# Performance work log

Measured on AMD Instinct MI355X. Metric: run time of the kernel, lower is better.

The kernel has to match this reference:

```python
import jax, jax.numpy as jnp
import numpy as np

DRUG_NUM, DIS_NUM, HIDE_DIM = 60000, 40000, 128
HOPS, N_LAYERS, N_HEADS, FFN_DIM, N_EDGES = 7, 2, 4, 512, 800000
N_NODES = DRUG_NUM + DIS_NUM


def _ln(x, s, b, eps=1e-5):
    m = jnp.mean(x, axis=-1, keepdims=True)
    v = jnp.var(x, axis=-1, keepdims=True)
    return (x - m) * jax.lax.rsqrt(v + eps) * s + b


def setup_inputs() -> dict:
    ks = jax.random.split(jax.random.key(0), 16)
    L, D, F = N_LAYERS, HIDE_DIM, FFN_DIM
    sd = 0.05  # param init scale
    n = lambda k, shape, s=sd: jax.random.normal(k, shape, jnp.float32) * s
    kk = jax.random.split(ks[15], 12)
    return {
        'ifTraining': 0,
        'uid': jax.random.randint(ks[0], (256,), 0, DRUG_NUM, jnp.int64 if jax.config.jax_enable_x64 else jnp.int32),
        'iid': jax.random.randint(ks[1], (256,), 0, DIS_NUM, jnp.int64 if jax.config.jax_enable_x64 else jnp.int32),
        'norm': 1,
        'drug_emb': n(ks[2], (DRUG_NUM, D), 0.1),
        'dis_emb': n(ks[3], (DIS_NUM, D), 0.1),
        'edge_src': jax.random.randint(ks[4], (N_EDGES,), 0, N_NODES, jnp.int32),
        'edge_dst': jax.random.randint(ks[5], (N_EDGES,), 0, N_NODES, jnp.int32),
        'edge_val': jax.random.uniform(ks[6], (N_EDGES,), jnp.float32) * 0.1,  # normalized adj values
        'att_w': n(ks[7], (D, D)), 'att_b': jnp.zeros((D,), jnp.float32),
        'ln1_s': jnp.ones((L, D), jnp.float32), 'ln1_b': jnp.zeros((L, D), jnp.float32),
        'q_w': n(kk[0], (L, D, D)), 'q_b': jnp.zeros((L, D), jnp.float32),
        'k_w': n(kk[1], (L, D, D)), 'k_b': jnp.zeros((L, D), jnp.float32),
        'v_w': n(kk[2], (L, D, D)), 'v_b': jnp.zeros((L, D), jnp.float32),
        'o_w': n(kk[3], (L, D, D)), 'o_b': jnp.zeros((L, D), jnp.float32),
        'ln2_s': jnp.ones((L, D), jnp.float32), 'ln2_b': jnp.zeros((L, D), jnp.float32),
        'f1_w': n(kk[4], (L, D, F)), 'f1_b': jnp.zeros((L, F), jnp.float32),
        'f2_w': n(kk[5], (L, F, D)), 'f2_b': jnp.zeros((L, D), jnp.float32),
        'fln_s': jnp.ones((D,), jnp.float32), 'fln_b': jnp.zeros((D,), jnp.float32),
        'attn_w': n(kk[6], (2 * D, 1)), 'attn_b': jnp.zeros((1,), jnp.float32),
    }


def reference(ifTraining, uid, iid, norm, drug_emb, dis_emb, edge_src, edge_dst, edge_val,
              att_w, att_b, ln1_s, ln1_b, q_w, q_b, k_w, k_b, v_w, v_b, o_w, o_b,
              ln2_s, ln2_b, f1_w, f1_b, f2_w, f2_b, fln_s, fln_b, attn_w, attn_b):
    N, D, S, dh = N_NODES, HIDE_DIM, HOPS + 1, HIDE_DIM // N_HEADS
    # ---- re_features: K sparse-adjacency hops over concatenated embeddings ----
    x = jnp.concatenate([drug_emb, dis_emb], axis=0)  # [N, D]
    feats = [x]
    for _ in range(HOPS):
        msgs = x[edge_src] * edge_val[:, None]          # [E, D] gather
        x = jax.ops.segment_sum(msgs, edge_dst, num_segments=N)  # [N, D] scatter-add
        feats.append(x)
    nf = jnp.stack(feats, axis=1)                        # [N, S, D]
    # ---- graph-transformer over the hop sequence (eval: dropout = identity) ----
    h = nf @ att_w + att_b                               # [N, S, D]
    for l in range(N_LAYERS):
        y = _ln(h, ln1_s[l], ln1_b[l])
        q = (y @ q_w[l] + q_b[l]).reshape(N, S, N_HEADS, dh)
        k = (y @ k_w[l] + k_b[l]).reshape(N, S, N_HEADS, dh)
        v = (y @ v_w[l] + v_b[l]).reshape(N, S, N_HEADS, dh)
        a = jnp.einsum('nshd,nthd->nhst', q, k) * (dh ** -0.5)
        a = jax.nn.softmax(a, axis=-1)                   # [N, H, S, S]
        y = jnp.einsum('nhst,nthd->nshd', a, v).reshape(N, S, D)
        h = h + (y @ o_w[l] + o_b[l])
        y = _ln(h, ln2_s[l], ln2_b[l])
        h = h + (jax.nn.gelu(y @ f1_w[l] + f1_b[l]) @ f2_w[l] + f2_b[l])
    out = _ln(h, fln_s, fln_b)
    # ---- readout: node token + softmax attention over hop tokens ----
    node = out[:, 0, :]                                  # [N, D]
    neigh = out[:, 1:, :]                                # [N, HOPS, D]
    target = jnp.broadcast_to(node[:, None, :], neigh.shape)
    att = jnp.concatenate([target, neigh], axis=-1) @ attn_w + attn_b  # [N, HOPS, 1]
    att = jax.nn.softmax(att, axis=1)
    final = node + jnp.sum(neigh * att, axis=1)          # [N, D]
    return final[:DRUG_NUM], final[DRUG_NUM:]
```

## Files before the change

kernel.cpp:

```cpp
#include <hip/hip_runtime.h>
#include <hip/hip_bf16.h>

typedef __hip_bfloat16 bf16;
typedef __attribute__((ext_vector_type(8))) short s16x8;
typedef __attribute__((ext_vector_type(4))) float f32x4;

#define NDRUG 60000
#define NDIS  40000
#define NN    100000
#define DIM   128
#define NHOPS 7
#define NEDGE 800000
#define NSB   98

__device__ __forceinline__ float u2f(unsigned short u) {
    union { unsigned int i; float f; } c; c.i = ((unsigned int)u) << 16; return c.f;
}
__device__ __forceinline__ ushort f2u(float f) {
    bf16 h = __float2bfloat16(f);
    return *reinterpret_cast<ushort*>(&h);
}


__global__ void k_init(const float* __restrict__ drug, const float* __restrict__ dis,
                       ushort* __restrict__ nf) {
    int i = blockIdx.x * 256 + threadIdx.x;
    if (i >= NN * 32) return;
    int n = i >> 5, g = (i & 31) << 2;
    const float* sp = (n < NDRUG) ? drug + (size_t)n * 128 + g
                                  : dis + (size_t)(n - NDRUG) * 128 + g;
    float4 v = *(const float4*)sp;
    ushort4 o;
    o.x = f2u(v.x); o.y = f2u(v.y); o.z = f2u(v.z); o.w = f2u(v.w);
    *(ushort4*)(nf + (size_t)n * 1024 + g) = o;
}

__global__ void k_count(const int* __restrict__ edst, int* __restrict__ cnt) {
    int e = blockIdx.x * 256 + threadIdx.x;
    if (e < NEDGE) atomicAdd(&cnt[edst[e]], 1);
}

__global__ void k_scanA(const int* __restrict__ cnt, int* __restrict__ incl,
                        int* __restrict__ btot) {
    __shared__ int part[1024];
    int b = blockIdx.x, t = threadIdx.x;
    int i = b * 1024 + t;
    part[t] = (i < NN) ? cnt[i] : 0;
    __syncthreads();
    for (int o = 1; o < 1024; o <<= 1) {
        int u = (t >= o) ? part[t - o] : 0;
        __syncthreads();
        part[t] += u;
        __syncthreads();
    }
    if (i < NN) incl[i] = part[t];
    if (t == 1023) btot[b] = part[1023];
}

__global__ void k_scanB(const int* __restrict__ btot, int* __restrict__ boff) {
    if (threadIdx.x == 0) {
        int run = 0;
        for (int b = 0; b < NSB; b++) { boff[b] = run; run += btot[b]; }
        boff[NSB] = run;
    }
}

__global__ void k_scanC(const int* __restrict__ cnt, const int* __restrict__ incl,
                        const int* __restrict__ boff, int* __restrict__ rp) {
    int i = blockIdx.x * 256 + threadIdx.x;
    if (i < NN) rp[i] = incl[i] - cnt[i] + boff[i >> 10];
    if (i == 0) rp[NN] = boff[NSB];
}

__global__ void k_copyrp(const int* __restrict__ rp, int* __restrict__ cur) {
    int i = blockIdx.x * 256 + threadIdx.x;
    if (i < NN) cur[i] = rp[i];
}

__global__ void k_scatter(const int* __restrict__ esrc, const int* __restrict__ edst,
                          const float* __restrict__ eval, int* __restrict__ cur,
                          int* __restrict__ ssrc, float* __restrict__ sval) {
    int e = blockIdx.x * 256 + threadIdx.x;
    if (e >= NEDGE) return;
    int d = edst[e];
    int pos = atomicAdd(&cur[d], 1);
    ssrc[pos] = esrc[e];
    sval[pos] = eval[e];
}

__global__ void k_hopg(ushort* __restrict__ nf, const int* __restrict__ rp,
                       const int* __restrict__ ssrc, const float* __restrict__ sval, int s) {
    int t = blockIdx.x * 256 + threadIdx.x;
    if (t >= NN * 32) return;
    int n = t >> 5, d0 = (t & 31) << 2;
    int e0 = rp[n], e1 = rp[n + 1];
    float4 a = make_float4(0.f, 0.f, 0.f, 0.f);
    for (int e = e0; e < e1; e++) {
        int src = ssrc[e];
        float val = sval[e];
        ushort4 u = *(const ushort4*)(nf + (size_t)src * 1024 + (size_t)(s - 1) * 128 + d0);
        a.x += u2f(u.x) * val; a.y += u2f(u.y) * val;
        a.z += u2f(u.z) * val; a.w += u2f(u.w) * val;
    }
    ushort4 o;
    o.x = f2u(a.x); o.y = f2u(a.y); o.z = f2u(a.z); o.w = f2u(a.w);
    *(ushort4*)(nf + (size_t)n * 1024 + (size_t)s * 128 + d0) = o;
}


__global__ void k_pack(const float* __restrict__ W, ushort* __restrict__ P, int K, int Nout) {
    int idx = blockIdx.x * 256 + threadIdx.x;
    int tot = (Nout >> 4) * (K >> 3) * 16;
    if (idx >= tot) return;
    int c = idx & 15;
    int r = idx >> 4;
    int kb = r % (K >> 3);
    int nt = r / (K >> 3);
    ushort o[8];
    #pragma unroll
    for (int i = 0; i < 8; i++)
        o[i] = f2u(W[(size_t)(kb * 8 + i) * Nout + nt * 16 + c]);
    uint4 v;
    v.x = (uint)o[0] | ((uint)o[1] << 16);
    v.y = (uint)o[2] | ((uint)o[3] << 16);
    v.z = (uint)o[4] | ((uint)o[5] << 16);
    v.w = (uint)o[6] | ((uint)o[7] << 16);
    *(uint4*)(P + (size_t)idx * 8) = v;
}

__global__ void k_catb(const float* __restrict__ qb, const float* __restrict__ kb,
                       const float* __restrict__ vb, float* __restrict__ o) {
    int i = threadIdx.x;
    o[i] = (i < 128) ? qb[i] : ((i < 256) ? kb[i - 128] : vb[i - 256]);
}


template <int ACT, int ADD, int OUTBF, int NTPW>
__global__ void k_mgemm(const ushort* __restrict__ X, const ushort* __restrict__ Wp,
                        const float* __restrict__ bias, void* __restrict__ Yv,
                        int M, int K, int Nout) {
    int w = threadIdx.x >> 6, lane = threadIdx.x & 63;
    int lr = lane & 15, lg = lane >> 4;
    int m0 = blockIdx.x * 16;
    int kb8 = K >> 3;
    int row = m0 + lr; if (row > M - 1) row = M - 1;
    const ushort* ap = X + (size_t)row * K + lg * 8;
    f32x4 acc[NTPW] = {};
    for (int k0 = 0; k0 < K; k0 += 32, ap += 32) {
        s16x8 af = *(const s16x8*)ap;
        int kb = (k0 >> 3) + lg;
        #pragma unroll
        for (int t = 0; t < NTPW; t++) {
            int nt = w + t * 4;
            const ushort* bp = Wp + (((size_t)nt * kb8 + kb) * 16 + lr) * 8;
            s16x8 bf_ = *(const s16x8*)bp;
            acc[t] = __builtin_amdgcn_mfma_f32_16x16x32_bf16(af, bf_, acc[t], 0, 0, 0);
        }
    }
    #pragma unroll
    for (int t = 0; t < NTPW; t++) {
        int n = (w + t * 4) * 16 + lr;
        float bv = bias[n];
        #pragma unroll
        for (int j = 0; j < 4; j++) {
            int m = m0 + lg * 4 + j;
            if (m >= M) continue;
            float v = acc[t][j] + bv;
            if (ACT == 1) {
                float x = v;
                float z = 0.7978845608028654f * (x + 0.044715f * x * x * x);
                v = x / (1.0f + __expf(-2.0f * z));
            }
            if (OUTBF) {
                ((ushort*)Yv)[(size_t)m * Nout + n] = f2u(v);
            } else if (ADD) {
                ((float*)Yv)[(size_t)m * Nout + n] += v;
            } else {
                ((float*)Yv)[(size_t)m * Nout + n] = v;
            }
        }
    }
}


__global__ void k_lnqkvattnO(float* __restrict__ H, const ushort* __restrict__ Wqkv,
                             const ushort* __restrict__ Wo, const float* __restrict__ sc,
                             const float* __restrict__ bi, const float* __restrict__ bqkv,
                             const float* __restrict__ bo, int M) {
    __shared__ ushort ylds[16][136];
    __shared__ ushort big[16][392];
    __shared__ float  as_[2][256];
    int w = threadIdx.x >> 6, lane = threadIdx.x & 63;
    int lr = lane & 15, lg = lane >> 4;
    int m0 = blockIdx.x * 16;

    #pragma unroll
    for (int i = 0; i < 4; i++) {
        int row = w * 4 + i;
        int grow = m0 + row; if (grow > M - 1) grow = M - 1;
        float2 x = *(const float2*)(H + (size_t)grow * 128 + lane * 2);
        float sum = x.x + x.y, sq = x.x * x.x + x.y * x.y;
        #pragma unroll
        for (int o = 32; o; o >>= 1) { sum += __shfl_xor(sum, o); sq += __shfl_xor(sq, o); }
        float mean = sum * (1.f / 128.f);
        float inv = rsqrtf(sq * (1.f / 128.f) - mean * mean + 1e-5f);
        float y0 = (x.x - mean) * inv * sc[lane * 2 + 0] + bi[lane * 2 + 0];
        float y1 = (x.y - mean) * inv * sc[lane * 2 + 1] + bi[lane * 2 + 1];
        *(uint*)&ylds[row][lane * 2] = (uint)f2u(y0) | ((uint)f2u(y1) << 16);
    }
    __syncthreads();

    {
        f32x4 acc[6] = {};
        for (int k0 = 0; k0 < 128; k0 += 32) {
            s16x8 af = *(const s16x8*)&ylds[lr][lg * 8 + k0];
            int kb = (k0 >> 3) + lg;
            #pragma unroll
            for (int t = 0; t < 6; t++) {
                int nt = w + t * 4;
                const ushort* bp = Wqkv + (((size_t)nt * 16 + kb) * 16 + lr) * 8;
                s16x8 bf_ = *(const s16x8*)bp;
                acc[t] = __builtin_amdgcn_mfma_f32_16x16x32_bf16(af, bf_, acc[t], 0, 0, 0);
            }
        }
        #pragma unroll
        for (int t = 0; t < 6; t++) {
            int n = (w + t * 4) * 16 + lr;
            float bv = bqkv[n];
            #pragma unroll
            for (int j = 0; j < 4; j++) big[lg * 4 + j][n] = f2u(acc[t][j] + bv);
        }
    }
    __syncthreads();

    if (w < 2) {
        int hh = lane >> 4, s_ = (lane >> 1) & 7, p = lane & 1;
        const float scale = 0.17677669529663687f;
        float dots[4];
        float mx = -1e30f;
        #pragma unroll
        for (int t4 = 0; t4 < 4; t4++) {
            int t = p * 4 + t4;
            float dot = 0.f;
            #pragma unroll
            for (int d = 0; d < 32; d++)
                dot += u2f(big[w * 8 + s_][hh * 32 + d]) * u2f(big[w * 8 + t][128 + hh * 32 + d]);
            dots[t4] = dot * scale;
            mx = fmaxf(mx, dots[t4]);
        }
        mx = fmaxf(mx, __shfl_xor(mx, 1));
        float sum = 0.f, e4[4];
        #pragma unroll
        for (int t4 = 0; t4 < 4; t4++) { e4[t4] = __expf(dots[t4] - mx); sum += e4[t4]; }
        sum += __shfl_xor(sum, 1);
        float rinv = 1.f / sum;
        #pragma unroll
        for (int t4 = 0; t4 < 4; t4++) as_[w][hh * 64 + s_ * 8 + p * 4 + t4] = e4[t4] * rinv;
    }
    __syncthreads();

    if (w < 2) {
        #pragma unroll
        for (int i = 0; i < 16; i++) {
            int o = i * 64 + lane;
            int ss = o >> 7, rem = o & 127, h2 = rem >> 5, dd = rem & 31;
            float accv = 0.f;
            #pragma unroll
            for (int t = 0; t < 8; t++)
                accv += as_[w][h2 * 64 + ss * 8 + t] * u2f(big[w * 8 + t][256 + h2 * 32 + dd]);
            ylds[w * 8 + ss][rem] = f2u(accv);
        }
    }
    __syncthreads();

    {
        f32x4 acc[2] = {};
        for (int k0 = 0; k0 < 128; k0 += 32) {
            s16x8 af = *(const s16x8*)&ylds[lr][lg * 8 + k0];
            int kb = (k0 >> 3) + lg;
            #pragma unroll
            for (int t = 0; t < 2; t++) {
                int nt = w + t * 4;
                const ushort* bp = Wo + (((size_t)nt * 16 + kb) * 16 + lr) * 8;
                s16x8 bf_ = *(const s16x8*)bp;
                acc[t] = __builtin_amdgcn_mfma_f32_16x16x32_bf16(af, bf_, acc[t], 0, 0, 0);
            }
        }
        #pragma unroll
        for (int t = 0; t < 2; t++) {
            int n = (w + t * 4) * 16 + lr;
            float bv = bo[n];
            #pragma unroll
            for (int j = 0; j < 4; j++) {
                int m = m0 + lg * 4 + j;
                if (m >= M) continue;
                H[(size_t)m * 128 + n] += acc[t][j] + bv;
            }
        }
    }
}


__global__ void k_lnffn(float* __restrict__ H, const ushort* __restrict__ Wf1,
                        const ushort* __restrict__ Wf2, const float* __restrict__ sc,
                        const float* __restrict__ bi, const float* __restrict__ b1,
                        const float* __restrict__ b2, int M) {
    __shared__ ushort ylds[16][136];
    __shared__ ushort big[16][520];
    int w = threadIdx.x >> 6, lane = threadIdx.x & 63;
    int lr = lane & 15, lg = lane >> 4;
    int m0 = blockIdx.x * 16;

    #pragma unroll
    for (int i = 0; i < 4; i++) {
        int row = w * 4 + i;
        int grow = m0 + row; if (grow > M - 1) grow = M - 1;
        float2 x = *(const float2*)(H + (size_t)grow * 128 + lane * 2);
        float sum = x.x + x.y, sq = x.x * x.x + x.y * x.y;
        #pragma unroll
        for (int o = 32; o; o >>= 1) { sum += __shfl_xor(sum, o); sq += __shfl_xor(sq, o); }
        float mean = sum * (1.f / 128.f);
        float inv = rsqrtf(sq * (1.f / 128.f) - mean * mean + 1e-5f);
        float y0 = (x.x - mean) * inv * sc[lane * 2 + 0] + bi[lane * 2 + 0];
        float y1 = (x.y - mean) * inv * sc[lane * 2 + 1] + bi[lane * 2 + 1];
        *(uint*)&ylds[row][lane * 2] = (uint)f2u(y0) | ((uint)f2u(y1) << 16);
    }
    __syncthreads();

    {
        f32x4 acc[8] = {};
        for (int k0 = 0; k0 < 128; k0 += 32) {
            s16x8 af = *(const s16x8*)&ylds[lr][lg * 8 + k0];
            int kb = (k0 >> 3) + lg;
            #pragma unroll
            for (int t = 0; t < 8; t++) {
                int nt = w + t * 4;
                const ushort* bp = Wf1 + (((size_t)nt * 16 + kb) * 16 + lr) * 8;
                s16x8 bf_ = *(const s16x8*)bp;
                acc[t] = __builtin_amdgcn_mfma_f32_16x16x32_bf16(af, bf_, acc[t], 0, 0, 0);
            }
        }
        #pragma unroll
        for (int t = 0; t < 8; t++) {
            int n = (w + t * 4) * 16 + lr;
            float bv = b1[n];
            #pragma unroll
            for (int j = 0; j < 4; j++) {
                float x = acc[t][j] + bv;
                float z = 0.7978845608028654f * (x + 0.044715f * x * x * x);
                big[lg * 4 + j][n] = f2u(x / (1.0f + __expf(-2.0f * z)));
            }
        }
    }
    __syncthreads();

    {
        f32x4 acc[2] = {};
        for (int k0 = 0; k0 < 512; k0 += 32) {
            s16x8 af = *(const s16x8*)&big[lr][lg * 8 + k0];
            int kb = (k0 >> 3) + lg;
            #pragma unroll
            for (int t = 0; t < 2; t++) {
                int nt = w + t * 4;
                const ushort* bp = Wf2 + (((size_t)nt * 64 + kb) * 16 + lr) * 8;
                s16x8 bf_ = *(const s16x8*)bp;
                acc[t] = __builtin_amdgcn_mfma_f32_16x16x32_bf16(af, bf_, acc[t], 0, 0, 0);
            }
        }
        #pragma unroll
        for (int t = 0; t < 2; t++) {
            int n = (w + t * 4) * 16 + lr;
            float bv = b2[n];
            #pragma unroll
            for (int j = 0; j < 4; j++) {
                int m = m0 + lg * 4 + j;
                if (m >= M) continue;
                H[(size_t)m * 128 + n] += acc[t][j] + bv;
            }
        }
    }
}


__global__ void k_pool(const float* __restrict__ Hc, const float* __restrict__ fs,
                       const float* __restrict__ fb, const float* __restrict__ aw,
                       const float* __restrict__ ab, float* __restrict__ out,
                       int Nc, int n0g) {
    int w = threadIdx.x >> 6, lane = threadIdx.x & 63;
    int nl = blockIdx.x * 4 + w;
    if (nl >= Nc) return;
    const float* hp = Hc + (size_t)nl * 1024;
    float s0 = fs[lane * 2], s1 = fs[lane * 2 + 1];
    float b0 = fb[lane * 2], b1 = fb[lane * 2 + 1];
    float2 yl[8];
    #pragma unroll
    for (int s = 0; s < 8; s++) {
        float2 x = *(const float2*)(hp + s * DIM + lane * 2);
        float sum = x.x + x.y, sq = x.x * x.x + x.y * x.y;
        #pragma unroll
        for (int o = 32; o; o >>= 1) { sum += __shfl_xor(sum, o); sq += __shfl_xor(sq, o); }
        float mean = sum * (1.f / 128.f);
        float inv = rsqrtf(sq * (1.f / 128.f) - mean * mean + 1e-5f);
        yl[s].x = (x.x - mean) * inv * s0 + b0;
        yl[s].y = (x.y - mean) * inv * s1 + b1;
    }
    float awn0 = aw[lane * 2], awn1 = aw[lane * 2 + 1];
    float awh0 = aw[128 + lane * 2], awh1 = aw[128 + lane * 2 + 1];
    float abv = ab[0];
    float lg[7];
    #pragma unroll
    for (int s = 0; s < 7; s++) {
        float part = yl[0].x * awn0 + yl[0].y * awn1 + yl[s + 1].x * awh0 + yl[s + 1].y * awh1;
        #pragma unroll
        for (int o = 32; o; o >>= 1) part += __shfl_xor(part, o);
        lg[s] = part + abv;
    }
    float mx = lg[0];
    #pragma unroll
    for (int s = 1; s < 7; s++) mx = fmaxf(mx, lg[s]);
    float sum = 0.f;
    #pragma unroll
    for (int s = 0; s < 7; s++) { lg[s] = __expf(lg[s] - mx); sum += lg[s]; }
    float rinv = 1.f / sum;
    float2 f = yl[0];
    #pragma unroll
    for (int s = 0; s < 7; s++) { f.x += lg[s] * rinv * yl[s + 1].x; f.y += lg[s] * rinv * yl[s + 1].y; }
    size_t ob = (size_t)(n0g + nl) * DIM + lane * 2;
    out[ob + 0] = f.x;
    out[ob + 1] = f.y;
}


extern "C" void kernel_launch(void* const* d_in, const int* in_sizes, int n_in,
                              void* d_out, int out_size, void* d_ws, size_t ws_size,
                              hipStream_t stream) {
    const float* drug  = (const float*)d_in[4];
    const float* dis   = (const float*)d_in[5];
    const int*   esrc  = (const int*)d_in[6];
    const int*   edst  = (const int*)d_in[7];
    const float* eval  = (const float*)d_in[8];
    const float* att_w = (const float*)d_in[9];
    const float* att_b = (const float*)d_in[10];
    const float* ln1_s = (const float*)d_in[11];
    const float* ln1_b = (const float*)d_in[12];
    const float* q_w   = (const float*)d_in[13];
    const float* q_b   = (const float*)d_in[14];
    const float* k_w   = (const float*)d_in[15];
    const float* k_b   = (const float*)d_in[16];
    const float* v_w   = (const float*)d_in[17];
    const float* v_b   = (const float*)d_in[18];
    const float* o_w   = (const float*)d_in[19];
    const float* o_b   = (const float*)d_in[20];
    const float* ln2_s = (const float*)d_in[21];
    const float* ln2_b = (const float*)d_in[22];
    const float* f1_w  = (const float*)d_in[23];
    const float* f1_b  = (const float*)d_in[24];
    const float* f2_w  = (const float*)d_in[25];
    const float* f2_b  = (const float*)d_in[26];
    const float* fln_s = (const float*)d_in[27];
    const float* fln_b = (const float*)d_in[28];
    const float* aw    = (const float*)d_in[29];
    const float* ab    = (const float*)d_in[30];
    float* out = (float*)d_out;

    char* ws = (char*)d_ws;
    size_t nfB = (size_t)NN * 1024 * 2;
    ushort* nf = (ushort*)ws;
    size_t off = (nfB + 255) & ~(size_t)255;

    ushort* wpk = (ushort*)(ws + off);
    size_t offCsr = off + (1 << 20);
    int*   rp   = (int*)(ws + offCsr);
    int*   cnt  = rp + (NN + 1);
    int*   ssrc = cnt + NN;
    float* sval = (float*)(ssrc + NEDGE);
    int*   incl = (int*)(sval + NEDGE);
    int*   btot = incl + NN;
    int*   boff = btot + 128;
    size_t csrInts = (size_t)(NN + 1) + NN + NEDGE + NEDGE + NN + 256;
    size_t off2 = offCsr + ((csrInts * 4 + 255) & ~(size_t)255);

    size_t scratchB = (ws_size > off2) ? ws_size - off2 : 0;
    long long ncMax = (long long)(scratchB / 4096);
    ncMax &= ~1LL;
    if (ncMax < 2) ncMax = 2;
    int Nc = (int)((ncMax < NN) ? ncMax : NN);
    int nchunks = (NN + Nc - 1) / Nc;
    Nc = (NN + nchunks - 1) / nchunks;
    if (Nc & 1) Nc++;
    size_t U = (size_t)Nc * 4096;
    float* hbuf = (float*)(ws + off2);

    size_t wpAtt = 0;
    size_t wpQKV[2], wpO[2], wpF1[2], wpF2[2];
    {
        size_t p = 16384;
        for (int l = 0; l < 2; l++) {
            wpQKV[l] = p; p += 49152;
            wpO[l]   = p; p += 16384;
            wpF1[l]  = p; p += 65536;
            wpF2[l]  = p; p += 65536;
        }
    }
    float* qkvB = (float*)(wpk + 409600);

    {
        int b128 = (16384 / 8 + 255) / 256;
        int b512 = (65536 / 8 + 255) / 256;
        k_pack<<<b128, 256, 0, stream>>>(att_w, wpk + wpAtt, 128, 128);
        for (int l = 0; l < 2; l++) {
            k_pack<<<b128, 256, 0, stream>>>(q_w + (size_t)l * 16384, wpk + wpQKV[l], 128, 128);
            k_pack<<<b128, 256, 0, stream>>>(k_w + (size_t)l * 16384, wpk + wpQKV[l] + 16384, 128, 128);
            k_pack<<<b128, 256, 0, stream>>>(v_w + (size_t)l * 16384, wpk + wpQKV[l] + 32768, 128, 128);
            k_pack<<<b128, 256, 0, stream>>>(o_w + (size_t)l * 16384, wpk + wpO[l], 128, 128);
            k_pack<<<b512, 256, 0, stream>>>(f1_w + (size_t)l * 65536, wpk + wpF1[l], 128, 512);
            k_pack<<<b512, 256, 0, stream>>>(f2_w + (size_t)l * 65536, wpk + wpF2[l], 512, 128);
            k_catb<<<1, 384, 0, stream>>>(q_b + l * 128, k_b + l * 128, v_b + l * 128, qkvB + l * 384);
        }
    }

    (void)hipMemsetAsync(cnt, 0, (size_t)NN * 4, stream);
    k_count<<<(NEDGE + 255) / 256, 256, 0, stream>>>(edst, cnt);
    k_scanA<<<NSB, 1024, 0, stream>>>(cnt, incl, btot);
    k_scanB<<<1, 64, 0, stream>>>(btot, boff);
    k_scanC<<<(NN + 255) / 256, 256, 0, stream>>>(cnt, incl, boff, rp);
    k_copyrp<<<(NN + 255) / 256, 256, 0, stream>>>(rp, cnt);
    k_scatter<<<(NEDGE + 255) / 256, 256, 0, stream>>>(esrc, edst, eval, cnt, ssrc, sval);

    k_init<<<(NN * 32 + 255) / 256, 256, 0, stream>>>(drug, dis, nf);
    for (int s = 1; s <= NHOPS; s++)
        k_hopg<<<(NN * 32 + 255) / 256, 256, 0, stream>>>(nf, rp, ssrc, sval, s);

    for (int c = 0; c < nchunks; c++) {
        int cn0 = c * Nc;
        int cn = NN - cn0; if (cn > Nc) cn = Nc;
        if (cn <= 0) break;
        int Mc = cn * 8;
        int mb = (Mc + 15) / 16;
        int nb = (cn + 3) / 4;

        k_mgemm<0, 0, 0, 2><<<mb, 256, 0, stream>>>(nf + (size_t)cn0 * 1024, wpk + wpAtt,
                                                    att_b, hbuf, Mc, 128, 128);
        for (int l = 0; l < 2; l++) {
            k_lnqkvattnO<<<mb, 256, 0, stream>>>(hbuf, wpk + wpQKV[l], wpk + wpO[l],
                                                 ln1_s + l * 128, ln1_b + l * 128,
                                                 qkvB + l * 384, o_b + l * 128, Mc);
            k_lnffn<<<mb, 256, 0, stream>>>(hbuf, wpk + wpF1[l], wpk + wpF2[l],
                                            ln2_s + l * 128, ln2_b + l * 128,
                                            f1_b + l * 512, f2_b + l * 128, Mc);
        }
        k_pool<<<nb, 256, 0, stream>>>(hbuf, fln_s, fln_b, aw, ab, out, cn, cn0);
    }
    (void)in_sizes; (void)n_in; (void)out_size;
}
```

Measured before the change: 3.045 ms.

## Fuse attention and FFN sublayers into one per-layer kernel with LDS-resident residual

Merges the LN+QKV+attention+O kernel and the LN+FFN kernel into a single k_layer kernel. Each block loads its 16 residual rows into shared memory once, applies both sublayer residual updates there, and writes them back once. This removes one launch per layer and the global round trip of the residual stream between the two sublayers. In exchange, shared memory per block grows (an extra 16x132 float tile and a larger big buffer), which may lower occupancy.

```diff
diff --git a/kernel.cpp b/kernel.cpp
--- a/kernel.cpp
+++ b/kernel.cpp
@@ -183,29 +183,43 @@
 }
 
 
-__global__ void k_lnqkvattnO(float* __restrict__ H, const ushort* __restrict__ Wqkv,
-                             const ushort* __restrict__ Wo, const float* __restrict__ sc,
-                             const float* __restrict__ bi, const float* __restrict__ bqkv,
-                             const float* __restrict__ bo, int M) {
+__global__ void k_layer(float* __restrict__ H,
+                        const ushort* __restrict__ Wqkv, const ushort* __restrict__ Wo,
+                        const ushort* __restrict__ Wf1, const ushort* __restrict__ Wf2,
+                        const float* __restrict__ s1v, const float* __restrict__ b1v,
+                        const float* __restrict__ bqkv, const float* __restrict__ bo,
+                        const float* __restrict__ s2v, const float* __restrict__ b2v,
+                        const float* __restrict__ bf1, const float* __restrict__ bf2,
+                        int M) {
+    __shared__ float  h[16][132];
     __shared__ ushort ylds[16][136];
-    __shared__ ushort big[16][392];
+    __shared__ ushort big[16][520];
     __shared__ float  as_[2][256];
-    int w = threadIdx.x >> 6, lane = threadIdx.x & 63;
+    int tid = threadIdx.x;
+    int w = tid >> 6, lane = tid & 63;
     int lr = lane & 15, lg = lane >> 4;
     int m0 = blockIdx.x * 16;
 
     #pragma unroll
+    for (int i = 0; i < 2; i++) {
+        int gi = i * 256 + tid;
+        int row = gi >> 5, c4 = (gi & 31) << 2;
+        int grow = m0 + row; if (grow > M - 1) grow = M - 1;
+        *(float4*)&h[row][c4] = *(const float4*)(H + (size_t)grow * 128 + c4);
+    }
+    __syncthreads();
+
+    #pragma unroll
     for (int i = 0; i < 4; i++) {
         int row = w * 4 + i;
-        int grow = m0 + row; if (grow > M - 1) grow = M - 1;
-        float2 x = *(const float2*)(H + (size_t)grow * 128 + lane * 2);
+        float2 x = *(const float2*)&h[row][lane * 2];
         float sum = x.x + x.y, sq = x.x * x.x + x.y * x.y;
         #pragma unroll
         for (int o = 32; o; o >>= 1) { sum += __shfl_xor(sum, o); sq += __shfl_xor(sq, o); }
         float mean = sum * (1.f / 128.f);
         float inv = rsqrtf(sq * (1.f / 128.f) - mean * mean + 1e-5f);
-        float y0 = (x.x - mean) * inv * sc[lane * 2 + 0] + bi[lane * 2 + 0];
-        float y1 = (x.y - mean) * inv * sc[lane * 2 + 1] + bi[lane * 2 + 1];
+        float y0 = (x.x - mean) * inv * s1v[lane * 2 + 0] + b1v[lane * 2 + 0];
+        float y1 = (x.y - mean) * inv * s1v[lane * 2 + 1] + b1v[lane * 2 + 1];
         *(uint*)&ylds[row][lane * 2] = (uint)f2u(y0) | ((uint)f2u(y1) << 16);
     }
     __syncthreads();
@@ -291,38 +305,22 @@
             int n = (w + t * 4) * 16 + lr;
             float bv = bo[n];
             #pragma unroll
-            for (int j = 0; j < 4; j++) {
-                int m = m0 + lg * 4 + j;
-                if (m >= M) continue;
-                H[(size_t)m * 128 + n] += acc[t][j] + bv;
-            }
-        }
-    }
-}
-
-
-__global__ void k_lnffn(float* __restrict__ H, const ushort* __restrict__ Wf1,
-                        const ushort* __restrict__ Wf2, const float* __restrict__ sc,
-                        const float* __restrict__ bi, const float* __restrict__ b1,
-                        const float* __restrict__ b2, int M) {
-    __shared__ ushort ylds[16][136];
-    __shared__ ushort big[16][520];
-    int w = threadIdx.x >> 6, lane = threadIdx.x & 63;
-    int lr = lane & 15, lg = lane >> 4;
-    int m0 = blockIdx.x * 16;
+            for (int j = 0; j < 4; j++) h[lg * 4 + j][n] += acc[t][j] + bv;
+        }
+    }
+    __syncthreads();
 
     #pragma unroll
     for (int i = 0; i < 4; i++) {
         int row = w * 4 + i;
-        int grow = m0 + row; if (grow > M - 1) grow = M - 1;
-        float2 x = *(const float2*)(H + (size_t)grow * 128 + lane * 2);
+        float2 x = *(const float2*)&h[row][lane * 2];
         float sum = x.x + x.y, sq = x.x * x.x + x.y * x.y;
         #pragma unroll
         for (int o = 32; o; o >>= 1) { sum += __shfl_xor(sum, o); sq += __shfl_xor(sq, o); }
         float mean = sum * (1.f / 128.f);
         float inv = rsqrtf(sq * (1.f / 128.f) - mean * mean + 1e-5f);
-        float y0 = (x.x - mean) * inv * sc[lane * 2 + 0] + bi[lane * 2 + 0];
-        float y1 = (x.y - mean) * inv * sc[lane * 2 + 1] + bi[lane * 2 + 1];
+        float y0 = (x.x - mean) * inv * s2v[lane * 2 + 0] + b2v[lane * 2 + 0];
+        float y1 = (x.y - mean) * inv * s2v[lane * 2 + 1] + b2v[lane * 2 + 1];
         *(uint*)&ylds[row][lane * 2] = (uint)f2u(y0) | ((uint)f2u(y1) << 16);
     }
     __syncthreads();
@@ -343,7 +341,7 @@
         #pragma unroll
         for (int t = 0; t < 8; t++) {
             int n = (w + t * 4) * 16 + lr;
-            float bv = b1[n];
+            float bv = bf1[n];
             #pragma unroll
             for (int j = 0; j < 4; j++) {
                 float x = acc[t][j] + bv;
@@ -370,14 +368,19 @@
         #pragma unroll
         for (int t = 0; t < 2; t++) {
             int n = (w + t * 4) * 16 + lr;
-            float bv = b2[n];
-            #pragma unroll
-            for (int j = 0; j < 4; j++) {
-                int m = m0 + lg * 4 + j;
-                if (m >= M) continue;
-                H[(size_t)m * 128 + n] += acc[t][j] + bv;
-            }
-        }
+            float bv = bf2[n];
+            #pragma unroll
+            for (int j = 0; j < 4; j++) h[lg * 4 + j][n] += acc[t][j] + bv;
+        }
+    }
+    __syncthreads();
+
+    #pragma unroll
+    for (int i = 0; i < 2; i++) {
+        int gi = i * 256 + tid;
+        int row = gi >> 5, c4 = (gi & 31) << 2;
+        int grow = m0 + row;
+        if (grow < M) *(float4*)(H + (size_t)grow * 128 + c4) = *(const float4*)&h[row][c4];
     }
 }
 
@@ -488,7 +491,6 @@
     int nchunks = (NN + Nc - 1) / Nc;
     Nc = (NN + nchunks - 1) / nchunks;
     if (Nc & 1) Nc++;
-    size_t U = (size_t)Nc * 4096;
     float* hbuf = (float*)(ws + off2);
 
     size_t wpAtt = 0;
@@ -542,10 +544,10 @@
         k_mgemm<0, 0, 0, 2><<<mb, 256, 0, stream>>>(nf + (size_t)cn0 * 1024, wpk + wpAtt,
                                                     att_b, hbuf, Mc, 128, 128);
         for (int l = 0; l < 2; l++) {
-            k_lnqkvattnO<<<mb, 256, 0, stream>>>(hbuf, wpk + wpQKV[l], wpk + wpO[l],
-                                                 ln1_s + l * 128, ln1_b + l * 128,
-                                                 qkvB + l * 384, o_b + l * 128, Mc);
-            k_lnffn<<<mb, 256, 0, stream>>>(hbuf, wpk + wpF1[l], wpk + wpF2[l],
+            k_layer<<<mb, 256, 0, stream>>>(hbuf, wpk + wpQKV[l], wpk + wpO[l],
+                                            wpk + wpF1[l], wpk + wpF2[l],
+                                            ln1_s + l * 128, ln1_b + l * 128,
+                                            qkvB + l * 384, o_b + l * 128,
                                             ln2_s + l * 128, ln2_b + l * 128,
                                             f1_b + l * 512, f2_b + l * 128, Mc);
         }
```

Measured after the change: 2.957 ms. -2.9%, faster.
